# Optimization experiments

Hardware: AMD Instinct MI355X
Metric: run time of the kernel (lower is better)

Reference implementation:

```python
import jax, jax.numpy as jnp
import numpy as np

B, C_IN, N = 64, 1, 8192
WIDTH, MODES, NLAYERS = 64, 16, 4


def setup_inputs() -> dict:
    key = jax.random.key(0)
    ks = jax.random.split(key, 10)
    scale = 1.0 / (WIDTH * WIDTH)
    inp = {
        "x": jax.random.normal(ks[0], (B, C_IN, N), dtype=jnp.float32),
        # lifting p: Linear(2, width)
        "p_w": jax.random.normal(ks[1], (WIDTH, 2), dtype=jnp.float32) * 0.5,
        "p_b": jax.random.normal(ks[2], (WIDTH,), dtype=jnp.float32) * 0.1,
        # 4 spectral conv weights, complex stored as real/imag (uniform like torch.rand cfloat)
        "sc_wr": scale * jax.random.uniform(ks[3], (NLAYERS, WIDTH, WIDTH, MODES), dtype=jnp.float32),
        "sc_wi": scale * jax.random.uniform(ks[4], (NLAYERS, WIDTH, WIDTH, MODES), dtype=jnp.float32),
        # 4 pointwise (1x1) conv weights/biases
        "w_w": jax.random.normal(ks[5], (NLAYERS, WIDTH, WIDTH), dtype=jnp.float32) / np.sqrt(WIDTH),
        "w_b": jax.random.normal(ks[6], (NLAYERS, WIDTH), dtype=jnp.float32) * 0.1,
        # projection q: Linear(width, 1)
        "q_w": jax.random.normal(ks[7], (1, WIDTH), dtype=jnp.float32) / np.sqrt(WIDTH),
        "q_b": jax.random.normal(ks[8], (1,), dtype=jnp.float32) * 0.1,
    }
    return inp


def spectral_conv(x, wr, wi, n):
    # x: [b, i, n] real; weights complex [i, o, modes]
    x_ft = jnp.fft.rfft(x, axis=-1)                      # [b, i, n//2+1] complex
    w = (wr + 1j * wi).astype(jnp.complex64)
    out_modes = jnp.einsum('bix,iox->box', x_ft[:, :, :MODES], w)
    out_ft = jnp.zeros((x.shape[0], w.shape[1], n // 2 + 1), dtype=jnp.complex64)
    out_ft = out_ft.at[:, :, :MODES].set(out_modes)
    return jnp.fft.irfft(out_ft, n=n, axis=-1)


def reference(x, p_w, p_b, sc_wr, sc_wi, w_w, w_b, q_w, q_b):
    b, _, n = x.shape
    grid = jnp.broadcast_to(jnp.linspace(0.0, 1.0, n, dtype=jnp.float32)[None, None, :], (b, 1, n))
    h = jnp.concatenate([x, grid], axis=1)               # [b, 2, n]
    # lifting: Linear over channel dim
    h = jnp.einsum('bcn,wc->bwn', h, p_w) + p_b[None, :, None]
    for l in range(NLAYERS):
        x1 = spectral_conv(h, sc_wr[l], sc_wi[l], n)
        x2 = jnp.einsum('bin,oi->bon', h, w_w[l]) + w_b[l][None, :, None]
        h = jax.nn.gelu(x1 + x2, approximate=False)
    out = jnp.einsum('bwn,ow->bon', h, q_w) + q_b[None, :, None]  # [b, 1, n]
    return out
```

## Files before the change

kernel.cpp:

```cpp
#include <hip/hip_runtime.h>
#include <math.h>


typedef _Float16 f16;
typedef _Float16 f16x2 __attribute__((ext_vector_type(2)));
typedef _Float16 f16x4 __attribute__((ext_vector_type(4)));
typedef _Float16 f16x8 __attribute__((ext_vector_type(8)));
typedef float    f32x2 __attribute__((ext_vector_type(2)));
typedef float    f32x4 __attribute__((ext_vector_type(4)));
typedef unsigned int u32;

#define BB 64
#define NN 8192

#define HT_S 64
#define HO_S 136

__device__ __forceinline__ int ht_swz(int n) { return ((n & 7) ^ ((n >> 3) & 7)) << 3; }

__device__ __forceinline__ float gelu_f(float v) {
    float x  = v * 0.70710678118654752f;
    float ax = fabsf(x);
    float t  = __builtin_amdgcn_rcpf(fmaf(0.3275911f, ax, 1.0f));
    float p  = fmaf(1.061405429f, t, -1.453152027f);
    p = fmaf(p, t, 1.421413741f);
    p = fmaf(p, t, -0.284496736f);
    p = fmaf(p, t, 0.254829592f);
    p = p * t;
    float e  = __expf(-x * x);
    float er = fmaf(-p, e, 1.0f);
    er = copysignf(er, x);
    return 0.5f * fmaf(v, er, v);
}

__global__ __launch_bounds__(256) void fill_basis(f16* __restrict__ basF,
                                                  f16* __restrict__ basI,
                                                  const float* __restrict__ w_w,
                                                  f16* __restrict__ Wh,
                                                  float* __restrict__ Sz) {
    int n = blockIdx.x * 256 + threadIdx.x;
    f16 row[32];
#pragma unroll
    for (int k = 0; k < 16; ++k) {
        float s, c;
        sincospif((float)(k * n) * (1.0f / 4096.0f), &s, &c);
        basF[k * NN + n]        = (f16)c;
        basF[(16 + k) * NN + n] = (f16)(-s);
        row[2 * k]     = (f16)c;
        row[2 * k + 1] = (f16)s;
    }
#pragma unroll
    for (int q = 0; q < 4; ++q) *(f16x8*)&basI[n * 32 + 8 * q] = *(f16x8*)&row[8 * q];
    Wh[n]        = (f16)w_w[n];
    Wh[n + 8192] = (f16)w_w[n + 8192];
    f32x4* S4 = (f32x4*)Sz;
    f32x4 z = {0.f, 0.f, 0.f, 0.f};
#pragma unroll
    for (int u = 0; u < 4; ++u) S4[n * 4 + u] = z;
}

__global__ __launch_bounds__(1024) void mode_mix(float* __restrict__ S,
                                                 const float* __restrict__ wr,
                                                 const float* __restrict__ wi,
                                                 f16* __restrict__ Mph) {
    int b = blockIdx.x, t = threadIdx.x;
    __shared__ float Ss[32 * 66];
    if (t < 512) {
        f32x4 v = *(const f32x4*)&S[b * 2048 + t * 4];
        int rw = t >> 4, cl = (t & 15) * 4;
#pragma unroll
        for (int e = 0; e < 4; ++e) Ss[rw * 66 + cl + e] = v[e];
    }
    __syncthreads();
    *(f32x2*)&S[b * 2048 + t * 2] = (f32x2){0.f, 0.f};

    int o = t >> 4, k = t & 15;
    const float* wrp = wr + o * 16 + k;
    const float* wip = wi + o * 16 + k;
    float ar = 0.f, ai = 0.f;
#pragma unroll 8
    for (int i = 0; i < 64; ++i) {
        float sr = Ss[k * 66 + i], si = Ss[(16 + k) * 66 + i];
        float wrv = wrp[i * 1024];
        float wiv = wip[i * 1024];
        ar = fmaf(sr, wrv, ar); ar = fmaf(-si, wiv, ar);
        ai = fmaf(sr, wiv, ai); ai = fmaf(si, wrv, ai);
    }
    float sc = (k == 0 ? 1.0f : 2.0f) * (1.0f / 8192.0f);
    f16x2 outv = { (f16)(sc * ar), (f16)(-sc * ai) };
    *(f16x2*)&Mph[b * 2048 + o * 32 + 2 * k] = outv;
}

__device__ __forceinline__ void dft_accum_g(const f16* Hout, const f16* __restrict__ basF_g,
                                            int n0, f32x4 sacc[2], int lane, int wv) {
    int q = lane >> 4, l15 = lane & 15;
    int o = (wv << 4) + l15;
#pragma unroll
    for (int ks = 0; ks < 4; ++ks) {
        f16x8 bh = *(const f16x8*)&Hout[o * HO_S + ks * 32 + q * 8];
#pragma unroll
        for (int mt = 0; mt < 2; ++mt) {
            f16x8 af = *(const f16x8*)&basF_g[(mt * 16 + l15) * NN + n0 + ks * 32 + q * 8];
            sacc[mt] = __builtin_amdgcn_mfma_f32_16x16x32_f16(af, bh, sacc[mt], 0, 0, 0);
        }
    }
}

__device__ __forceinline__ void dft_flush(const f32x4 sacc[2], float* __restrict__ S,
                                          int b, int lane, int wv) {
    int q = lane >> 4, l15 = lane & 15;
#pragma unroll
    for (int mt = 0; mt < 2; ++mt)
#pragma unroll
        for (int r = 0; r < 4; ++r)
            atomicAdd(&S[(b * 32 + mt * 16 + q * 4 + r) * 64 + (wv << 4) + l15],
                      sacc[mt][r]);
}

__global__ __launch_bounds__(256, 3) void lift_kernel(const float* __restrict__ x,
                                                      const float* __restrict__ p_w,
                                                      const float* __restrict__ p_b,
                                                      f16* __restrict__ h,
                                                      const f16* __restrict__ basF_g,
                                                      float* __restrict__ S) {
    __shared__ f16 Hout[64 * HO_S];
    int t = threadIdx.x;
    int b = blockIdx.x >> 5;
    int g = blockIdx.x & 31;
    int lane = t & 63, wv = t >> 6;
    int ns = (t & 15) << 3;

    float w0[4], w1[4], pb[4];
#pragma unroll
    for (int r = 0; r < 4; ++r) {
        int o = (t >> 4) + 16 * r;
        w0[r] = p_w[2 * o]; w1[r] = p_w[2 * o + 1]; pb[r] = p_b[o];
    }

    f32x4 X[2][2];
#pragma unroll
    for (int tile = 0; tile < 2; ++tile) {
        int n0 = ((g << 1) + tile) << 7;
        X[tile][0] = *(const f32x4*)&x[(b << 13) + n0 + ns];
        X[tile][1] = *(const f32x4*)&x[(b << 13) + n0 + ns + 4];
    }

    f32x4 sacc[2] = {{0.f,0.f,0.f,0.f},{0.f,0.f,0.f,0.f}};
#pragma unroll
    for (int tile = 0; tile < 2; ++tile) {
        int n0 = ((g << 1) + tile) << 7;
#pragma unroll
        for (int r = 0; r < 4; ++r) {
            int o = (t >> 4) + 16 * r;
            f16 vals[8];
#pragma unroll
            for (int j = 0; j < 8; ++j) {
                int n = n0 + ns + j;
                float xv = X[tile][j >> 2][j & 3];
                vals[j] = (f16)(w0[r] * xv + w1[r] * ((float)n * (1.0f / 8191.0f)) + pb[r]);
            }
            *(f16x8*)&Hout[o * HO_S + ns] = *(f16x8*)vals;
            *(f16x8*)(h + (((size_t)(b * 64 + o)) << 13) + n0 + ns) = *(f16x8*)vals;
        }
        __syncthreads();
        dft_accum_g(Hout, basF_g, n0, sacc, lane, wv);
        if (tile == 0) __syncthreads();
    }
    dft_flush(sacc, S, b, lane, wv);
}

template <int DO_DFT>
__global__ __launch_bounds__(256, 3) void layer_kernel(f16* __restrict__ h,
                                                       const f16* __restrict__ Wl_h,
                                                       const float* __restrict__ bl,
                                                       const f16* __restrict__ Mph,
                                                       const f16* __restrict__ basF_g,
                                                       const f16* __restrict__ basI_g,
                                                       float* __restrict__ S,
                                                       const float* __restrict__ q_w,
                                                       const float* __restrict__ q_b,
                                                       float* __restrict__ out) {
    __shared__ __align__(16) f16 Ht[128 * HT_S];
    __shared__ __align__(16) f16 Hout[DO_DFT ? 64 * HO_S : 8];
    __shared__ float bls[64];
    int t = threadIdx.x;
    int b = blockIdx.x >> 5;
    int g = blockIdx.x & 31;
    f16* hbase = h + (((size_t)(b * 64)) << 13);
    int lane = t & 63, wv = t >> 6;
    int q = lane >> 4, l15 = lane & 15;
    int blk = t >> 1, half = t & 1;
    int ig = blk >> 4, nb = blk & 15;
    int i0 = ig << 3, nst = nb << 3;
    int swz = nb & 7;
    int n0_0 = (g << 1) << 7, n0_1 = ((g << 1) + 1) << 7;
    f16* hbt0 = hbase + n0_0;
    f16* hbt1 = hbase + n0_1;

    f16x8 Bw[4][2], Bm[4];
#pragma unroll
    for (int ct = 0; ct < 4; ++ct) {
#pragma unroll
        for (int ks = 0; ks < 2; ++ks)
            Bw[ct][ks] = *(const f16x8*)&Wl_h[(ct * 16 + l15) * 64 + ks * 32 + q * 8];
        Bm[ct] = *(const f16x8*)&Mph[b * 2048 + (ct * 16 + l15) * 32 + q * 8];
    }
    if (t < 64) bls[t] = bl[t];

    f16x8 R0[4];
#pragma unroll
    for (int k = 0; k < 4; ++k)
        R0[k] = *(const f16x8*)(hbt0 + ((size_t)(i0 + half * 4 + k) << 13) + nst);
    f16x8 Ab0[2];
#pragma unroll
    for (int mtl = 0; mtl < 2; ++mtl)
        Ab0[mtl] = *(const f16x8*)&basI_g[(size_t)(n0_0 + (2 * wv + mtl) * 16 + l15) * 32 + q * 8];
    {
        const u32* rd = (const u32*)R0;
#pragma unroll
        for (int j = 0; j < 8; ++j) {
            u32 sel = (j & 1) ? 0x07060302u : 0x05040100u;
            int jd = j >> 1;
            u32 oo[2] __attribute__((aligned(8)));
            oo[0] = __builtin_amdgcn_perm(rd[4 + jd],  rd[jd],      sel);
            oo[1] = __builtin_amdgcn_perm(rd[12 + jd], rd[8 + jd],  sel);
            int col = (i0 ^ ((j ^ swz) << 3)) + half * 4;
            *(f16x4*)&Ht[(nst + j) * HT_S + col] = *(const f16x4*)oo;
        }
    }
    __syncthreads();

    f16x8 R1[4];
#pragma unroll
    for (int k = 0; k < 4; ++k)
        R1[k] = *(const f16x8*)(hbt1 + ((size_t)(i0 + half * 4 + k) << 13) + nst);
    f16x8 Ab1[2];
#pragma unroll
    for (int mtl = 0; mtl < 2; ++mtl)
        Ab1[mtl] = *(const f16x8*)&basI_g[(size_t)(n0_1 + (2 * wv + mtl) * 16 + l15) * 32 + q * 8];

    float bv[4];
#pragma unroll
    for (int ct = 0; ct < 4; ++ct) bv[ct] = bls[ct * 16 + l15];

    f32x4 sacc[2] = {{0.f,0.f,0.f,0.f},{0.f,0.f,0.f,0.f}};

    f32x4 acc[4][2];
#pragma unroll
    for (int ct = 0; ct < 4; ++ct)
#pragma unroll
        for (int m = 0; m < 2; ++m) acc[ct][m] = (f32x4){0.f, 0.f, 0.f, 0.f};
#pragma unroll
    for (int mtl = 0; mtl < 2; ++mtl) {
        int nrow = (2 * wv + mtl) * 16 + l15;
        const f16* hrow = &Ht[nrow * HT_S];
        int g3 = ht_swz(nrow);
#pragma unroll
        for (int ks = 0; ks < 2; ++ks) {
            f16x8 Ah = *(const f16x8*)&hrow[(ks * 32 + q * 8) ^ g3];
#pragma unroll
            for (int ct = 0; ct < 4; ++ct)
                acc[ct][mtl] = __builtin_amdgcn_mfma_f32_16x16x32_f16(
                    Ah, Bw[ct][ks], acc[ct][mtl], 0, 0, 0);
        }
#pragma unroll
        for (int ct = 0; ct < 4; ++ct)
            acc[ct][mtl] = __builtin_amdgcn_mfma_f32_16x16x32_f16(
                Ab0[mtl], Bm[ct], acc[ct][mtl], 0, 0, 0);
    }

    if (DO_DFT) {
#pragma unroll
        for (int ct = 0; ct < 4; ++ct) {
            int o = ct * 16 + l15;
#pragma unroll
            for (int mtl = 0; mtl < 2; ++mtl) {
                int nbase = (2 * wv + mtl) * 16 + q * 4;
                float gg[4];
#pragma unroll
                for (int r = 0; r < 4; ++r)
                    gg[r] = gelu_f(acc[ct][mtl][r] + bv[ct]);
                f16x2 lo = __builtin_bit_cast(f16x2, __builtin_amdgcn_cvt_pkrtz(gg[0], gg[1]));
                f16x2 hi = __builtin_bit_cast(f16x2, __builtin_amdgcn_cvt_pkrtz(gg[2], gg[3]));
                f16x4 pk = {lo[0], lo[1], hi[0], hi[1]};
                *(f16x4*)&Hout[o * HO_S + nbase] = pk;
            }
        }
        __syncthreads();
#pragma unroll
        for (int r = 0; r < 4; ++r) {
            int o = (t >> 4) + 16 * r;
            int ns2 = (t & 15) << 3;
            *(f16x8*)(hbt0 + ((size_t)o << 13) + ns2) = *(f16x8*)&Hout[o * HO_S + ns2];
        }
        {
            const u32* rd = (const u32*)R1;
#pragma unroll
            for (int j = 0; j < 8; ++j) {
                u32 sel = (j & 1) ? 0x07060302u : 0x05040100u;
                int jd = j >> 1;
                u32 oo[2] __attribute__((aligned(8)));
                oo[0] = __builtin_amdgcn_perm(rd[4 + jd],  rd[jd],     sel);
                oo[1] = __builtin_amdgcn_perm(rd[12 + jd], rd[8 + jd], sel);
                int col = (i0 ^ ((j ^ swz) << 3)) + half * 4;
                *(f16x4*)&Ht[(nst + j) * HT_S + col] = *(const f16x4*)oo;
            }
        }
        dft_accum_g(Hout, basF_g, n0_0, sacc, lane, wv);
        __syncthreads();
    } else {
        float qv[4];
#pragma unroll
        for (int ct = 0; ct < 4; ++ct) qv[ct] = q_w[ct * 16 + l15];
        float part[2][4] = {{0.f,0.f,0.f,0.f},{0.f,0.f,0.f,0.f}};
#pragma unroll
        for (int ct = 0; ct < 4; ++ct)
#pragma unroll
            for (int mtl = 0; mtl < 2; ++mtl)
#pragma unroll
                for (int r = 0; r < 4; ++r)
                    part[mtl][r] = fmaf(qv[ct], gelu_f(acc[ct][mtl][r] + bv[ct]), part[mtl][r]);
#pragma unroll
        for (int mtl = 0; mtl < 2; ++mtl)
#pragma unroll
            for (int r = 0; r < 4; ++r) {
                float s = part[mtl][r];
#pragma unroll
                for (int m = 1; m < 16; m <<= 1) s += __shfl_xor(s, m, 64);
                if (l15 == 0)
                    out[(b << 13) + n0_0 + (2 * wv + mtl) * 16 + q * 4 + r] = s + q_b[0];
            }
        __syncthreads();
        {
            const u32* rd = (const u32*)R1;
#pragma unroll
            for (int j = 0; j < 8; ++j) {
                u32 sel = (j & 1) ? 0x07060302u : 0x05040100u;
                int jd = j >> 1;
                u32 oo[2] __attribute__((aligned(8)));
                oo[0] = __builtin_amdgcn_perm(rd[4 + jd],  rd[jd],     sel);
                oo[1] = __builtin_amdgcn_perm(rd[12 + jd], rd[8 + jd], sel);
                int col = (i0 ^ ((j ^ swz) << 3)) + half * 4;
                *(f16x4*)&Ht[(nst + j) * HT_S + col] = *(const f16x4*)oo;
            }
        }
        __syncthreads();
    }

#pragma unroll
    for (int ct = 0; ct < 4; ++ct)
#pragma unroll
        for (int m = 0; m < 2; ++m) acc[ct][m] = (f32x4){0.f, 0.f, 0.f, 0.f};
#pragma unroll
    for (int mtl = 0; mtl < 2; ++mtl) {
        int nrow = (2 * wv + mtl) * 16 + l15;
        const f16* hrow = &Ht[nrow * HT_S];
        int g3 = ht_swz(nrow);
#pragma unroll
        for (int ks = 0; ks < 2; ++ks) {
            f16x8 Ah = *(const f16x8*)&hrow[(ks * 32 + q * 8) ^ g3];
#pragma unroll
            for (int ct = 0; ct < 4; ++ct)
                acc[ct][mtl] = __builtin_amdgcn_mfma_f32_16x16x32_f16(
                    Ah, Bw[ct][ks], acc[ct][mtl], 0, 0, 0);
        }
#pragma unroll
        for (int ct = 0; ct < 4; ++ct)
            acc[ct][mtl] = __builtin_amdgcn_mfma_f32_16x16x32_f16(
                Ab1[mtl], Bm[ct], acc[ct][mtl], 0, 0, 0);
    }

    if (DO_DFT) {
#pragma unroll
        for (int ct = 0; ct < 4; ++ct) {
            int o = ct * 16 + l15;
#pragma unroll
            for (int mtl = 0; mtl < 2; ++mtl) {
                int nbase = (2 * wv + mtl) * 16 + q * 4;
                float gg[4];
#pragma unroll
                for (int r = 0; r < 4; ++r)
                    gg[r] = gelu_f(acc[ct][mtl][r] + bv[ct]);
                f16x2 lo = __builtin_bit_cast(f16x2, __builtin_amdgcn_cvt_pkrtz(gg[0], gg[1]));
                f16x2 hi = __builtin_bit_cast(f16x2, __builtin_amdgcn_cvt_pkrtz(gg[2], gg[3]));
                f16x4 pk = {lo[0], lo[1], hi[0], hi[1]};
                *(f16x4*)&Hout[o * HO_S + nbase] = pk;
            }
        }
        __syncthreads();
#pragma unroll
        for (int r = 0; r < 4; ++r) {
            int o = (t >> 4) + 16 * r;
            int ns2 = (t & 15) << 3;
            *(f16x8*)(hbt1 + ((size_t)o << 13) + ns2) = *(f16x8*)&Hout[o * HO_S + ns2];
        }
        dft_accum_g(Hout, basF_g, n0_1, sacc, lane, wv);
        dft_flush(sacc, S, b, lane, wv);
    } else {
        float qv[4];
#pragma unroll
        for (int ct = 0; ct < 4; ++ct) qv[ct] = q_w[ct * 16 + l15];
        float part[2][4] = {{0.f,0.f,0.f,0.f},{0.f,0.f,0.f,0.f}};
#pragma unroll
        for (int ct = 0; ct < 4; ++ct)
#pragma unroll
            for (int mtl = 0; mtl < 2; ++mtl)
#pragma unroll
                for (int r = 0; r < 4; ++r)
                    part[mtl][r] = fmaf(qv[ct], gelu_f(acc[ct][mtl][r] + bv[ct]), part[mtl][r]);
#pragma unroll
        for (int mtl = 0; mtl < 2; ++mtl)
#pragma unroll
            for (int r = 0; r < 4; ++r) {
                float s = part[mtl][r];
#pragma unroll
                for (int m = 1; m < 16; m <<= 1) s += __shfl_xor(s, m, 64);
                if (l15 == 0)
                    out[(b << 13) + n0_1 + (2 * wv + mtl) * 16 + q * 4 + r] = s + q_b[0];
            }
    }
}

extern "C" void kernel_launch(void* const* d_in, const int* in_sizes, int n_in,
                              void* d_out, int out_size, void* d_ws, size_t ws_size,
                              hipStream_t stream) {
    const float* x     = (const float*)d_in[0];
    const float* p_w   = (const float*)d_in[1];
    const float* p_b   = (const float*)d_in[2];
    const float* sc_wr = (const float*)d_in[3];
    const float* sc_wi = (const float*)d_in[4];
    const float* w_w   = (const float*)d_in[5];
    const float* w_b   = (const float*)d_in[6];
    const float* q_w   = (const float*)d_in[7];
    const float* q_b   = (const float*)d_in[8];
    float* out = (float*)d_out;

    char* ws = (char*)d_ws;
    f16*   h    = (f16*)ws;
    float* S    = (float*)(ws + 67108864ull);
    f16*   Mph  = (f16*)(ws + 67633152ull);
    f16*   basF = (f16*)(ws + 67895296ull);
    f16*   basI = (f16*)(ws + 68419584ull);
    f16*   Wh   = (f16*)(ws + 68943872ull);

    hipLaunchKernelGGL(fill_basis, dim3(NN / 256), dim3(256), 0, stream,
                       basF, basI, w_w, Wh, S);
    hipLaunchKernelGGL(lift_kernel, dim3(BB * 32), dim3(256), 0, stream,
                       x, p_w, p_b, h, basF, S);
    for (int l = 0; l < 4; ++l) {
        hipLaunchKernelGGL(mode_mix, dim3(BB), dim3(1024), 0, stream,
                           S, sc_wr + l * 65536, sc_wi + l * 65536, Mph);
        if (l < 3) {
            hipLaunchKernelGGL((layer_kernel<1>), dim3(BB * 32), dim3(256), 0, stream,
                               h, Wh + l * 4096, w_b + l * 64, Mph, basF, basI, S,
                               q_w, q_b, out);
        } else {
            hipLaunchKernelGGL((layer_kernel<0>), dim3(BB * 32), dim3(256), 0, stream,
                               h, Wh + l * 4096, w_b + l * 64, Mph, basF, basI, S,
                               q_w, q_b, out);
        }
    }
}
```

Measured before the change: 288.8 us.

## Alias Ht and Hout in shared pool; stage DFT basis in LDS for lift

In layer_kernel, the Ht and Hout shared buffers now share one pool, which cuts LDS per block and may let more blocks fit per CU. Extra barriers are added because the two buffers now overlap: one before each GELU write to Hout, and the first tile's DFT accumulation is moved ahead of the Ht restaging with a barrier in between. In lift_kernel, each tile's Fourier basis slice is staged cooperatively into LDS before the MFMA accumulation instead of being read directly from global memory. The cost is additional __syncthreads and less overlap between the DFT accumulation and the restaging work.

```diff
diff --git a/kernel.cpp b/kernel.cpp
--- a/kernel.cpp
+++ b/kernel.cpp
@@ -15,6 +15,7 @@
 
 #define HT_S 64
 #define HO_S 136
+#define BF_S 136
 
 __device__ __forceinline__ int ht_swz(int n) { return ((n & 7) ^ ((n >> 3) & 7)) << 3; }
 
@@ -91,6 +92,21 @@
     *(f16x2*)&Mph[b * 2048 + o * 32 + 2 * k] = outv;
 }
 
+__device__ __forceinline__ void dft_accum(const f16* Hout, const f16* BasF,
+                                          f32x4 sacc[2], int lane, int wv) {
+    int q = lane >> 4, l15 = lane & 15;
+    int o = (wv << 4) + l15;
+#pragma unroll
+    for (int ks = 0; ks < 4; ++ks) {
+        f16x8 bh = *(const f16x8*)&Hout[o * HO_S + ks * 32 + q * 8];
+#pragma unroll
+        for (int mt = 0; mt < 2; ++mt) {
+            f16x8 af = *(const f16x8*)&BasF[(mt * 16 + l15) * BF_S + ks * 32 + q * 8];
+            sacc[mt] = __builtin_amdgcn_mfma_f32_16x16x32_f16(af, bh, sacc[mt], 0, 0, 0);
+        }
+    }
+}
+
 __device__ __forceinline__ void dft_accum_g(const f16* Hout, const f16* __restrict__ basF_g,
                                             int n0, f32x4 sacc[2], int lane, int wv) {
     int q = lane >> 4, l15 = lane & 15;
@@ -124,6 +140,7 @@
                                                       const f16* __restrict__ basF_g,
                                                       float* __restrict__ S) {
     __shared__ f16 Hout[64 * HO_S];
+    __shared__ f16 BasF[32 * BF_S];
     int t = threadIdx.x;
     int b = blockIdx.x >> 5;
     int g = blockIdx.x & 31;
@@ -162,8 +179,13 @@
             *(f16x8*)&Hout[o * HO_S + ns] = *(f16x8*)vals;
             *(f16x8*)(h + (((size_t)(b * 64 + o)) << 13) + n0 + ns) = *(f16x8*)vals;
         }
-        __syncthreads();
-        dft_accum_g(Hout, basF_g, n0, sacc, lane, wv);
+#pragma unroll
+        for (int u = 0; u < 2; ++u) {
+            int km = t >> 3, nn = (t & 7) * 16 + u * 8;
+            *(f16x8*)&BasF[km * BF_S + nn] = *(const f16x8*)&basF_g[km * NN + n0 + nn];
+        }
+        __syncthreads();
+        dft_accum(Hout, BasF, sacc, lane, wv);
         if (tile == 0) __syncthreads();
     }
     dft_flush(sacc, S, b, lane, wv);
@@ -180,8 +202,9 @@
                                                        const float* __restrict__ q_w,
                                                        const float* __restrict__ q_b,
                                                        float* __restrict__ out) {
-    __shared__ __align__(16) f16 Ht[128 * HT_S];
-    __shared__ __align__(16) f16 Hout[DO_DFT ? 64 * HO_S : 8];
+    __shared__ __align__(16) char pool[DO_DFT ? 17408 : 16384];
+    f16* Ht   = (f16*)pool;
+    f16* Hout = (f16*)pool;
     __shared__ float bls[64];
     int t = threadIdx.x;
     int b = blockIdx.x >> 5;
@@ -270,6 +293,7 @@
     }
 
     if (DO_DFT) {
+        __syncthreads();
 #pragma unroll
         for (int ct = 0; ct < 4; ++ct) {
             int o = ct * 16 + l15;
@@ -293,6 +317,8 @@
             int ns2 = (t & 15) << 3;
             *(f16x8*)(hbt0 + ((size_t)o << 13) + ns2) = *(f16x8*)&Hout[o * HO_S + ns2];
         }
+        dft_accum_g(Hout, basF_g, n0_0, sacc, lane, wv);
+        __syncthreads();
         {
             const u32* rd = (const u32*)R1;
 #pragma unroll
@@ -306,7 +332,6 @@
                 *(f16x4*)&Ht[(nst + j) * HT_S + col] = *(const f16x4*)oo;
             }
         }
-        dft_accum_g(Hout, basF_g, n0_0, sacc, lane, wv);
         __syncthreads();
     } else {
         float qv[4];
@@ -371,6 +396,7 @@
     }
 
     if (DO_DFT) {
+        __syncthreads();
 #pragma unroll
         for (int ct = 0; ct < 4; ++ct) {
             int o = ct * 16 + l15;
```

New measurement: 293.2 us. About the same (+1.5%).
